# Performance work log

Measured on AMD Instinct MI355X. Metric: run time of the kernel, lower is better.

Reference implementation:

```python
import jax, jax.numpy as jnp
import numpy as np

N_ELEC = 64
IN_C = 64
HID = [64, 128]
OUT_C = 128
BATCH = 2048
BN_EPS = 1e-5


def build_graph():
    """Replicates EEGGraphNet._build_graph_structure with random 3D electrode positions."""
    rng = np.random.RandomState(0)
    pos = rng.rand(N_ELEC, 3).astype(np.float64)
    d = np.sqrt(((pos[:, None, :] - pos[None, :, :]) ** 2).sum(-1))
    thr = np.percentile(d[d > 0], 30)
    src, dst = [], []
    for i in range(N_ELEC):
        for j in range(i + 1, N_ELEC):
            if d[i, j] < thr:
                src += [i, j]
                dst += [j, i]
    return np.asarray(src, np.int32), np.asarray(dst, np.int32)


def setup_inputs() -> dict:
    key = jax.random.key(0)
    ks = jax.random.split(key, 8)
    src, dst = build_graph()
    dims = [IN_C] + HID + [OUT_C]  # [64, 64, 128, 128]
    inp = {"x": jax.random.normal(ks[0], (BATCH, N_ELEC, IN_C), jnp.float32)}
    for li in range(3):
        fi, fo = dims[li], dims[li + 1]
        inp[f"W{li+1}"] = jax.random.normal(ks[li + 1], (fi, fo), jnp.float32) * (1.0 / np.sqrt(fi))
        inp[f"b{li+1}"] = jnp.zeros((fo,), jnp.float32)
    for li in range(2):  # BN after first two convs
        inp[f"g{li+1}"] = jnp.ones((dims[li + 1],), jnp.float32)
        inp[f"be{li+1}"] = jnp.zeros((dims[li + 1],), jnp.float32)
    inp["src"] = jnp.asarray(src)
    inp["dst"] = jnp.asarray(dst)
    return inp


def gcn_conv(x, W, b, src, dst, edge_norm, self_norm):
    # x: (B, N, Fin) -> (B, N, Fout). GCN with self-loops, symmetric norm.
    h = jnp.einsum("bnf,fo->bno", x, W)
    msg = h[:, src, :] * edge_norm[None, :, None]          # (B, E, Fout) gather
    agg = jnp.zeros_like(h).at[:, dst, :].add(msg)         # scatter-add over dst
    return agg + h * self_norm[None, :, None] + b


def batchnorm(x, g, be):
    # torch BatchNorm1d over flattened (B*N, C) nodes, training-mode batch stats
    m = jnp.mean(x, axis=(0, 1))
    v = jnp.mean((x - m) ** 2, axis=(0, 1))
    return g * (x - m) * jax.lax.rsqrt(v + BN_EPS) + be


def reference(x, W1, b1, W2, b2, W3, b3, g1, be1, g2, be2, src, dst):
    # degree (with self-loop) is identical across graphs in the batch
    deg = jnp.zeros((N_ELEC,), x.dtype).at[dst].add(1.0) + 1.0
    inv_sqrt = jax.lax.rsqrt(deg)
    edge_norm = inv_sqrt[src] * inv_sqrt[dst]
    self_norm = 1.0 / deg

    h = gcn_conv(x, W1, b1, src, dst, edge_norm, self_norm)
    h = jax.nn.relu(batchnorm(h, g1, be1))
    h = gcn_conv(h, W2, b2, src, dst, edge_norm, self_norm)
    h = jax.nn.relu(batchnorm(h, g2, be2))
    h = gcn_conv(h, W3, b3, src, dst, edge_norm, self_norm)
    return jnp.mean(h, axis=1)  # global mean pool over electrodes -> (B, OUT_C)
```

## Files before the change

### kernel.cpp

```cpp
#include <hip/hip_runtime.h>
#include <hip/hip_bf16.h>

typedef unsigned short ushortT;
typedef unsigned int uintT;
typedef __attribute__((ext_vector_type(8))) short short8;
typedef __attribute__((ext_vector_type(4))) float f32x4;

#define BATCH   2048
#define NELEC   64
#define BN_EPS  1e-5f

#define OFF_AMEAN  4096
#define OFF_SS1    4160
#define OFF_SS2    4288
#define OFF_PS1    4544
#define OFF_PQ1    8640
#define OFF_PS2    12736
#define OFF_PQ2    20928
#define OFF_ABF    29120
#define OFF_W1T    33216
#define OFF_W2T    37312
#define OFF_H1     45504
#define OFF_T1     4239808
#define OFF_T2     4239808
#define OFF_H2     12628416

#define MFMA(a, b, c) __builtin_amdgcn_mfma_f32_16x16x32_bf16(a, b, c, 0, 0, 0)

__device__ inline float bf2f(ushortT u) { return __uint_as_float(((uintT)u) << 16); }
__device__ inline ushortT f2bf(float f) {
  uintT u = __float_as_uint(f);
  u = (u + 0x7FFFu + ((u >> 16) & 1u)) >> 16;
  return (ushortT)u;
}
__device__ inline void split2(float f, ushortT& hi, ushortT& lo) {
  hi = f2bf(f);
  lo = f2bf(f - bf2f(hi));
}
__device__ inline void splitT8(const float* f, short8& hi, short8& lo) {
  #pragma unroll
  for (int e = 0; e < 8; ++e) {
    uintT u = __float_as_uint(f[e]);
    float fh = __uint_as_float(u & 0xFFFF0000u);
    hi[e] = (short)(u >> 16);
    lo[e] = (short)f2bf(f[e] - fh);
  }
}

__global__ __launch_bounds__(256) void prep_kernel(const int* __restrict__ src,
    const int* __restrict__ dst, int E,
    const float* __restrict__ W1, const float* __restrict__ W2,
    float* __restrict__ ws) {
  __shared__ float degS[NELEC];
  __shared__ float As[NELEC * NELEC];
  int t = threadIdx.x;
  if (t < NELEC) degS[t] = 1.0f;
  for (int i = t; i < NELEC * NELEC; i += 256) As[i] = 0.0f;
  __syncthreads();
  for (int e = t; e < E; e += 256) atomicAdd(&degS[dst[e]], 1.0f);
  __syncthreads();
  for (int e = t; e < E; e += 256) {
    float en = rsqrtf(degS[src[e]]) * rsqrtf(degS[dst[e]]);
    atomicAdd(&As[dst[e] * NELEC + src[e]], en);
  }
  __syncthreads();
  if (t < NELEC) As[t * NELEC + t] += 1.0f / degS[t];
  __syncthreads();
  ushortT* abf = (ushortT*)(ws + OFF_ABF);
  for (int i = t; i < 4096; i += 256) {
    ushortT hi, lo; split2(As[i], hi, lo);
    abf[i] = hi; abf[4096 + i] = lo;
  }
  if (t < NELEC) {
    float s = 0.0f;
    for (int n = 0; n < NELEC; ++n) s += As[n * NELEC + t];
    ws[OFF_AMEAN + t] = s * (1.0f / NELEC);
  }
  ushortT* w1t = (ushortT*)(ws + OFF_W1T);
  for (int i = t; i < 4096; i += 256) {
    int o = i >> 6, k = i & 63;
    ushortT hi, lo; split2(W1[k * 64 + o], hi, lo);
    w1t[i] = hi; w1t[4096 + i] = lo;
  }
  ushortT* w2t = (ushortT*)(ws + OFF_W2T);
  for (int i = t; i < 8192; i += 256) {
    int o = i >> 6, k = i & 63;
    ushortT hi, lo; split2(W2[k * 128 + o], hi, lo);
    w2t[i] = hi; w2t[8192 + i] = lo;
  }
}

__global__ __launch_bounds__(256) void wgemm1_kernel(const float* __restrict__ x,
    float* __restrict__ ws) {
  const int t = threadIdx.x, w = t >> 6, lane = t & 63;
  const int c = lane & 15, g = lane >> 4;
  const int b = blockIdx.x * 4 + w;
  const ushortT* w1t = (const ushortT*)(ws + OFF_W1T);
  ushortT* t1 = (ushortT*)(ws + OFF_T1) + (size_t)b * 4096;

  short8 Xh[4][2], Xl[4][2];
  #pragma unroll
  for (int rt = 0; rt < 4; ++rt) {
    #pragma unroll
    for (int ks = 0; ks < 2; ++ks) {
      const float* p = x + (size_t)b * 4096 + (rt * 16 + c) * 64 + ks * 32 + g * 8;
      float4 fa = *(const float4*)p, fb = *(const float4*)(p + 4);
      float f[8] = {fa.x, fa.y, fa.z, fa.w, fb.x, fb.y, fb.z, fb.w};
      splitT8(f, Xh[rt][ks], Xl[rt][ks]);
    }
  }
  #pragma unroll
  for (int s = 0; s < 4; ++s) {
    f32x4 acc[4] = {{0,0,0,0},{0,0,0,0},{0,0,0,0},{0,0,0,0}};
    #pragma unroll
    for (int ks = 0; ks < 2; ++ks) {
      short8 bh = *(const short8*)(w1t + (s * 16 + c) * 64 + ks * 32 + g * 8);
      short8 bl = *(const short8*)(w1t + 4096 + (s * 16 + c) * 64 + ks * 32 + g * 8);
      #pragma unroll
      for (int rt = 0; rt < 4; ++rt) {
        acc[rt] = MFMA(Xh[rt][ks], bh, acc[rt]);
        acc[rt] = MFMA(Xh[rt][ks], bl, acc[rt]);
        acc[rt] = MFMA(Xl[rt][ks], bh, acc[rt]);
      }
    }
    #pragma unroll
    for (int rt = 0; rt < 4; ++rt) {
      uint2 pk;
      pk.x = (uintT)f2bf(acc[rt][0]) | ((uintT)f2bf(acc[rt][1]) << 16);
      pk.y = (uintT)f2bf(acc[rt][2]) | ((uintT)f2bf(acc[rt][3]) << 16);
      *(uint2*)(t1 + (s * 16 + c) * 64 + rt * 16 + 4 * g) = pk;
    }
  }
}

__global__ __launch_bounds__(256) void agemm1_kernel(const float* __restrict__ b1,
    float* __restrict__ ws) {
  const int t = threadIdx.x, w = t >> 6, lane = t & 63;
  const int c = lane & 15, g = lane >> 4;
  const int wg = blockIdx.x * 4 + w;
  const int ns = wg & 3;
  const int b0 = (wg >> 2) * 2;
  const ushortT* abf = (const ushortT*)(ws + OFF_ABF);
  short8 Bh[2], Bl[2];
  #pragma unroll
  for (int ks = 0; ks < 2; ++ks) {
    Bh[ks] = *(const short8*)(abf + (ns * 16 + c) * 64 + ks * 32 + g * 8);
    Bl[ks] = *(const short8*)(abf + 4096 + (ns * 16 + c) * 64 + ks * 32 + g * 8);
  }
  float Sa[4][4] = {}, Qa[4][4] = {};
  #pragma unroll
  for (int ib = 0; ib < 2; ++ib) {
    const int b = b0 + ib;
    const ushortT* t1 = (const ushortT*)(ws + OFF_T1) + (size_t)b * 4096;
    ushortT* h1 = (ushortT*)(ws + OFF_H1) + (size_t)b * 4096;
    #pragma unroll
    for (int rt = 0; rt < 4; ++rt) {
      f32x4 acc = {0, 0, 0, 0};
      #pragma unroll
      for (int ks = 0; ks < 2; ++ks) {
        short8 tf = *(const short8*)(t1 + (rt * 16 + c) * 64 + ks * 32 + g * 8);
        acc = MFMA(tf, Bh[ks], acc);
        acc = MFMA(tf, Bl[ks], acc);
      }
      float4 bv = *(const float4*)(b1 + rt * 16 + 4 * g);
      float v0 = acc[0] + bv.x, v1 = acc[1] + bv.y;
      float v2 = acc[2] + bv.z, v3 = acc[3] + bv.w;
      Sa[rt][0] += v0; Qa[rt][0] += v0 * v0;
      Sa[rt][1] += v1; Qa[rt][1] += v1 * v1;
      Sa[rt][2] += v2; Qa[rt][2] += v2 * v2;
      Sa[rt][3] += v3; Qa[rt][3] += v3 * v3;
      uint2 pk;
      pk.x = (uintT)f2bf(v0) | ((uintT)f2bf(v1) << 16);
      pk.y = (uintT)f2bf(v2) | ((uintT)f2bf(v3) << 16);
      *(uint2*)(h1 + (ns * 16 + c) * 64 + rt * 16 + 4 * g) = pk;
    }
  }
  const int slot = blockIdx.x & 63;
  #pragma unroll
  for (int rt = 0; rt < 4; ++rt) {
    #pragma unroll
    for (int r = 0; r < 4; ++r) {
      float S = Sa[rt][r], Q = Qa[rt][r];
      S += __shfl_xor(S, 1); S += __shfl_xor(S, 2);
      S += __shfl_xor(S, 4); S += __shfl_xor(S, 8);
      Q += __shfl_xor(Q, 1); Q += __shfl_xor(Q, 2);
      Q += __shfl_xor(Q, 4); Q += __shfl_xor(Q, 8);
      if (c == 0) {
        const int ch = rt * 16 + 4 * g + r;
        atomicAdd(&ws[OFF_PS1 + slot * 64 + ch], S);
        atomicAdd(&ws[OFF_PQ1 + slot * 64 + ch], Q);
      }
    }
  }
}

__global__ void reduce1_kernel(const float* __restrict__ g1, const float* __restrict__ be1,
                               float* __restrict__ ws) {
  int t = threadIdx.x;
  if (t < 64) {
    float S = 0.0f, Q = 0.0f;
    for (int s = 0; s < 64; ++s) { S += ws[OFF_PS1 + s * 64 + t]; Q += ws[OFF_PQ1 + s * 64 + t]; }
    const float inv = 1.0f / (float)(BATCH * NELEC);
    float m = S * inv;
    float v = fmaxf(Q * inv - m * m, 0.0f);
    float sc = g1[t] * rsqrtf(v + BN_EPS);
    ws[OFF_SS1 + t] = sc;
    ws[OFF_SS1 + 64 + t] = fmaf(-m, sc, be1[t]);
  }
}

__global__ void reduce2_kernel(const float* __restrict__ g2, const float* __restrict__ be2,
                               float* __restrict__ ws) {
  int t = threadIdx.x;
  if (t < 128) {
    float S = 0.0f, Q = 0.0f;
    for (int s = 0; s < 64; ++s) { S += ws[OFF_PS2 + s * 128 + t]; Q += ws[OFF_PQ2 + s * 128 + t]; }
    const float inv = 1.0f / (float)(BATCH * NELEC);
    float m = S * inv;
    float v = fmaxf(Q * inv - m * m, 0.0f);
    float sc = g2[t] * rsqrtf(v + BN_EPS);
    ws[OFF_SS2 + t] = sc;
    ws[OFF_SS2 + 128 + t] = fmaf(-m, sc, be2[t]);
  }
}

__global__ __launch_bounds__(256) void wgemm2_kernel(float* __restrict__ ws) {
  const int t = threadIdx.x, w = t >> 6, lane = t & 63;
  const int c = lane & 15, g = lane >> 4;
  const int b = blockIdx.x * 4 + w;
  const ushortT* w2t = (const ushortT*)(ws + OFF_W2T);
  const ushortT* h1 = (const ushortT*)(ws + OFF_H1) + (size_t)b * 4096;
  ushortT* t2 = (ushortT*)(ws + OFF_T2) + (size_t)b * 8192;

  float s1v[2][8], t1v[2][8];
  #pragma unroll
  for (int ks = 0; ks < 2; ++ks) {
    const float* sp = ws + OFF_SS1 + ks * 32 + g * 8;
    const float* tp = ws + OFF_SS1 + 64 + ks * 32 + g * 8;
    float4 sa = *(const float4*)sp, sb = *(const float4*)(sp + 4);
    float4 ta = *(const float4*)tp, tb = *(const float4*)(tp + 4);
    s1v[ks][0]=sa.x; s1v[ks][1]=sa.y; s1v[ks][2]=sa.z; s1v[ks][3]=sa.w;
    s1v[ks][4]=sb.x; s1v[ks][5]=sb.y; s1v[ks][6]=sb.z; s1v[ks][7]=sb.w;
    t1v[ks][0]=ta.x; t1v[ks][1]=ta.y; t1v[ks][2]=ta.z; t1v[ks][3]=ta.w;
    t1v[ks][4]=tb.x; t1v[ks][5]=tb.y; t1v[ks][6]=tb.z; t1v[ks][7]=tb.w;
  }
  short8 Yh[4][2], Yl[4][2];
  #pragma unroll
  for (int rt = 0; rt < 4; ++rt) {
    #pragma unroll
    for (int ks = 0; ks < 2; ++ks) {
      short8 hv = *(const short8*)(h1 + (rt * 16 + c) * 64 + ks * 32 + g * 8);
      float f[8];
      #pragma unroll
      for (int e = 0; e < 8; ++e)
        f[e] = fmaxf(fmaf(bf2f((ushortT)hv[e]), s1v[ks][e], t1v[ks][e]), 0.0f);
      splitT8(f, Yh[rt][ks], Yl[rt][ks]);
    }
  }
  #pragma unroll
  for (int s = 0; s < 8; ++s) {
    f32x4 acc[4] = {{0,0,0,0},{0,0,0,0},{0,0,0,0},{0,0,0,0}};
    #pragma unroll
    for (int ks = 0; ks < 2; ++ks) {
      short8 bh = *(const short8*)(w2t + (s * 16 + c) * 64 + ks * 32 + g * 8);
      short8 bl = *(const short8*)(w2t + 8192 + (s * 16 + c) * 64 + ks * 32 + g * 8);
      #pragma unroll
      for (int rt = 0; rt < 4; ++rt) {
        acc[rt] = MFMA(Yh[rt][ks], bh, acc[rt]);
        acc[rt] = MFMA(Yh[rt][ks], bl, acc[rt]);
        acc[rt] = MFMA(Yl[rt][ks], bh, acc[rt]);
      }
    }
    #pragma unroll
    for (int rt = 0; rt < 4; ++rt) {
      uint2 pk;
      pk.x = (uintT)f2bf(acc[rt][0]) | ((uintT)f2bf(acc[rt][1]) << 16);
      pk.y = (uintT)f2bf(acc[rt][2]) | ((uintT)f2bf(acc[rt][3]) << 16);
      *(uint2*)(t2 + (s * 16 + c) * 64 + rt * 16 + 4 * g) = pk;
    }
  }
}

__global__ __launch_bounds__(256) void agemm2_kernel(const float* __restrict__ b2,
    float* __restrict__ ws) {
  const int t = threadIdx.x, w = t >> 6, lane = t & 63;
  const int c = lane & 15, g = lane >> 4;
  const int wg = blockIdx.x * 4 + w;
  const int ns = wg & 3;
  const int b0 = (wg >> 2) * 2;
  const ushortT* abf = (const ushortT*)(ws + OFF_ABF);
  short8 Bh[2], Bl[2];
  #pragma unroll
  for (int ks = 0; ks < 2; ++ks) {
    Bh[ks] = *(const short8*)(abf + (ns * 16 + c) * 64 + ks * 32 + g * 8);
    Bl[ks] = *(const short8*)(abf + 4096 + (ns * 16 + c) * 64 + ks * 32 + g * 8);
  }
  float Sa[8][4] = {}, Qa[8][4] = {};
  #pragma unroll
  for (int ib = 0; ib < 2; ++ib) {
    const int b = b0 + ib;
    const ushortT* t2 = (const ushortT*)(ws + OFF_T2) + (size_t)b * 8192;
    ushortT* h2 = (ushortT*)(ws + OFF_H2) + (size_t)b * 8192;
    #pragma unroll
    for (int rt = 0; rt < 8; ++rt) {
      f32x4 acc = {0, 0, 0, 0};
      #pragma unroll
      for (int ks = 0; ks < 2; ++ks) {
        short8 tf = *(const short8*)(t2 + (rt * 16 + c) * 64 + ks * 32 + g * 8);
        acc = MFMA(tf, Bh[ks], acc);
        acc = MFMA(tf, Bl[ks], acc);
      }
      float4 bv = *(const float4*)(b2 + rt * 16 + 4 * g);
      float v0 = acc[0] + bv.x, v1 = acc[1] + bv.y;
      float v2 = acc[2] + bv.z, v3 = acc[3] + bv.w;
      Sa[rt][0] += v0; Qa[rt][0] += v0 * v0;
      Sa[rt][1] += v1; Qa[rt][1] += v1 * v1;
      Sa[rt][2] += v2; Qa[rt][2] += v2 * v2;
      Sa[rt][3] += v3; Qa[rt][3] += v3 * v3;
      uint2 pk;
      pk.x = (uintT)f2bf(v0) | ((uintT)f2bf(v1) << 16);
      pk.y = (uintT)f2bf(v2) | ((uintT)f2bf(v3) << 16);
      *(uint2*)(h2 + (ns * 16 + c) * 128 + rt * 16 + 4 * g) = pk;
    }
  }
  const int slot = blockIdx.x & 63;
  #pragma unroll
  for (int rt = 0; rt < 8; ++rt) {
    #pragma unroll
    for (int r = 0; r < 4; ++r) {
      float S = Sa[rt][r], Q = Qa[rt][r];
      S += __shfl_xor(S, 1); S += __shfl_xor(S, 2);
      S += __shfl_xor(S, 4); S += __shfl_xor(S, 8);
      Q += __shfl_xor(Q, 1); Q += __shfl_xor(Q, 2);
      Q += __shfl_xor(Q, 4); Q += __shfl_xor(Q, 8);
      if (c == 0) {
        const int ch = rt * 16 + 4 * g + r;
        atomicAdd(&ws[OFF_PS2 + slot * 128 + ch], S);
        atomicAdd(&ws[OFF_PQ2 + slot * 128 + ch], Q);
      }
    }
  }
}

__global__ __launch_bounds__(256) void layer3_kernel(const float* __restrict__ W3,
    const float* __restrict__ b3, const float* __restrict__ ws,
    float* __restrict__ out) {
  const int w = threadIdx.x >> 6, lane = threadIdx.x & 63;
  const int item = blockIdx.x * 4 + w;
  const int f0 = lane * 2;
  const float s2a = ws[OFF_SS2 + f0],       s2b = ws[OFF_SS2 + f0 + 1];
  const float t2a = ws[OFF_SS2 + 128 + f0], t2b = ws[OFF_SS2 + 128 + f0 + 1];
  const float* am = ws + OFF_AMEAN;
  const ushortT* h2 = (const ushortT*)(ws + OFF_H2) + (size_t)item * 8192;
  float v0 = 0.0f, v1 = 0.0f;
  #pragma unroll 8
  for (int m = 0; m < 64; ++m) {
    uintT pk = *(const uintT*)(h2 + m * 128 + f0);
    float y0 = fmaxf(fmaf(bf2f((ushortT)(pk & 0xffffu)), s2a, t2a), 0.0f);
    float y1 = fmaxf(fmaf(bf2f((ushortT)(pk >> 16)),     s2b, t2b), 0.0f);
    float a = am[m];
    v0 = fmaf(a, y0, v0);
    v1 = fmaf(a, y1, v1);
  }
  float o0 = b3[f0], o1 = b3[f0 + 1];
  #pragma unroll 8
  for (int k = 0; k < 128; ++k) {
    float vk = __shfl((k & 1) ? v1 : v0, k >> 1, 64);
    o0 = fmaf(vk, W3[k * 128 + f0],     o0);
    o1 = fmaf(vk, W3[k * 128 + f0 + 1], o1);
  }
  float2 ov; ov.x = o0; ov.y = o1;
  *(float2*)(out + (size_t)item * 128 + f0) = ov;
}

extern "C" void kernel_launch(void* const* d_in, const int* in_sizes, int n_in,
                              void* d_out, int out_size, void* d_ws, size_t ws_size,
                              hipStream_t stream) {
  const float* x   = (const float*)d_in[0];
  const float* W1  = (const float*)d_in[1];
  const float* b1  = (const float*)d_in[2];
  const float* W2  = (const float*)d_in[3];
  const float* b2  = (const float*)d_in[4];
  const float* W3  = (const float*)d_in[5];
  const float* b3  = (const float*)d_in[6];
  const float* g1  = (const float*)d_in[7];
  const float* be1 = (const float*)d_in[8];
  const float* g2  = (const float*)d_in[9];
  const float* be2 = (const float*)d_in[10];
  const int*   src = (const int*)d_in[11];
  const int*   dst = (const int*)d_in[12];
  const int E = in_sizes[11];
  float* ws  = (float*)d_ws;
  float* out = (float*)d_out;

  hipMemsetAsync((void*)(ws + OFF_PS1), 0, (size_t)(29120 - OFF_PS1) * 4, stream);
  hipLaunchKernelGGL(prep_kernel,   dim3(1),    dim3(256), 0, stream, src, dst, E, W1, W2, ws);
  hipLaunchKernelGGL(wgemm1_kernel, dim3(512),  dim3(256), 0, stream, x, ws);
  hipLaunchKernelGGL(agemm1_kernel, dim3(1024), dim3(256), 0, stream, b1, ws);
  hipLaunchKernelGGL(reduce1_kernel,dim3(1),    dim3(64),  0, stream, g1, be1, ws);
  hipLaunchKernelGGL(wgemm2_kernel, dim3(512),  dim3(256), 0, stream, ws);
  hipLaunchKernelGGL(agemm2_kernel, dim3(1024), dim3(256), 0, stream, b2, ws);
  hipLaunchKernelGGL(reduce2_kernel,dim3(1),    dim3(128), 0, stream, g2, be2, ws);
  hipLaunchKernelGGL(layer3_kernel, dim3(512),  dim3(256), 0, stream, W3, b3, ws, out);
}
```

Before: 225.0 us.

## Fuse weight GEMM and adjacency GEMM per layer through LDS staging

Merges the separate weight-GEMM and adjacency-GEMM kernels of layers 1 and 2 into single kernels. The intermediate X·W tile now stays in padded shared memory instead of going through global memory. Weights are loaded into LDS once per block, and operand layouts are padded to a row stride of 72 (136 for the H2 staging) to avoid bank conflicts. H1 and H2 are written back with coalesced 16-byte stores from LDS. This removes two kernel launches and a large global round-trip of the intermediates. In exchange it uses heavy LDS per block, which may limit occupancy.

```diff
diff --git a/kernel.cpp b/kernel.cpp
--- a/kernel.cpp
+++ b/kernel.cpp
@@ -17,13 +17,11 @@
 #define OFF_PQ1    8640
 #define OFF_PS2    12736
 #define OFF_PQ2    20928
-#define OFF_ABF    29120
-#define OFF_W1T    33216
-#define OFF_W2T    37312
-#define OFF_H1     45504
-#define OFF_T1     4239808
-#define OFF_T2     4239808
-#define OFF_H2     12628416
+#define UOFF_A     0
+#define UOFF_W1T   9216
+#define UOFF_W2T   18432
+#define UOFF_H1    36864
+#define UOFF_H2    (36864 + 8388608)
 
 #define MFMA(a, b, c) __builtin_amdgcn_mfma_f32_16x16x32_bf16(a, b, c, 0, 0, 0)
 
@@ -45,6 +43,12 @@
     hi[e] = (short)(u >> 16);
     lo[e] = (short)f2bf(f[e] - fh);
   }
+}
+__device__ inline uint2 pack4(f32x4 v) {
+  uint2 pk;
+  pk.x = (uintT)f2bf(v[0]) | ((uintT)f2bf(v[1]) << 16);
+  pk.y = (uintT)f2bf(v[2]) | ((uintT)f2bf(v[3]) << 16);
+  return pk;
 }
 
 __global__ __launch_bounds__(256) void prep_kernel(const int* __restrict__ src,
@@ -66,131 +70,146 @@
   __syncthreads();
   if (t < NELEC) As[t * NELEC + t] += 1.0f / degS[t];
   __syncthreads();
-  ushortT* abf = (ushortT*)(ws + OFF_ABF);
+  ushortT* U = (ushortT*)(ws + 29120);
+  ushortT* a72 = U + UOFF_A;
   for (int i = t; i < 4096; i += 256) {
+    int row = i >> 6, k = i & 63;
     ushortT hi, lo; split2(As[i], hi, lo);
-    abf[i] = hi; abf[4096 + i] = lo;
+    a72[row * 72 + k] = hi; a72[4608 + row * 72 + k] = lo;
   }
   if (t < NELEC) {
     float s = 0.0f;
     for (int n = 0; n < NELEC; ++n) s += As[n * NELEC + t];
     ws[OFF_AMEAN + t] = s * (1.0f / NELEC);
   }
-  ushortT* w1t = (ushortT*)(ws + OFF_W1T);
+  ushortT* w1t = U + UOFF_W1T;
   for (int i = t; i < 4096; i += 256) {
     int o = i >> 6, k = i & 63;
     ushortT hi, lo; split2(W1[k * 64 + o], hi, lo);
-    w1t[i] = hi; w1t[4096 + i] = lo;
-  }
-  ushortT* w2t = (ushortT*)(ws + OFF_W2T);
+    w1t[o * 72 + k] = hi; w1t[4608 + o * 72 + k] = lo;
+  }
+  ushortT* w2t = U + UOFF_W2T;
   for (int i = t; i < 8192; i += 256) {
     int o = i >> 6, k = i & 63;
     ushortT hi, lo; split2(W2[k * 128 + o], hi, lo);
-    w2t[i] = hi; w2t[8192 + i] = lo;
-  }
-}
-
-__global__ __launch_bounds__(256) void wgemm1_kernel(const float* __restrict__ x,
-    float* __restrict__ ws) {
-  const int t = threadIdx.x, w = t >> 6, lane = t & 63;
-  const int c = lane & 15, g = lane >> 4;
-  const int b = blockIdx.x * 4 + w;
-  const ushortT* w1t = (const ushortT*)(ws + OFF_W1T);
-  ushortT* t1 = (ushortT*)(ws + OFF_T1) + (size_t)b * 4096;
-
+    w2t[o * 72 + k] = hi; w2t[9216 + o * 72 + k] = lo;
+  }
+}
+
+__global__ __launch_bounds__(512, 2) void layer1_fused(const float* __restrict__ x,
+    const float* __restrict__ b1, float* __restrict__ ws) {
+  __shared__ ushortT Wl[9216];
+  __shared__ ushortT Tt[36864];
+  const int t = threadIdx.x;
+  ushortT* U = (ushortT*)(ws + 29120);
+  for (int i = t; i < 1152; i += 512)
+    ((uint4*)Wl)[i] = ((const uint4*)(U + UOFF_W1T))[i];
+  const int w = t >> 6, lane = t & 63, c = lane & 15, g = lane >> 4;
+  const int b = blockIdx.x * 8 + w;
   short8 Xh[4][2], Xl[4][2];
   #pragma unroll
-  for (int rt = 0; rt < 4; ++rt) {
-    #pragma unroll
-    for (int ks = 0; ks < 2; ++ks) {
-      const float* p = x + (size_t)b * 4096 + (rt * 16 + c) * 64 + ks * 32 + g * 8;
+  for (int nq = 0; nq < 4; ++nq) {
+    #pragma unroll
+    for (int ks = 0; ks < 2; ++ks) {
+      const float* p = x + (size_t)b * 4096 + (nq * 16 + c) * 64 + ks * 32 + g * 8;
       float4 fa = *(const float4*)p, fb = *(const float4*)(p + 4);
       float f[8] = {fa.x, fa.y, fa.z, fa.w, fb.x, fb.y, fb.z, fb.w};
-      splitT8(f, Xh[rt][ks], Xl[rt][ks]);
-    }
-  }
-  #pragma unroll
-  for (int s = 0; s < 4; ++s) {
-    f32x4 acc[4] = {{0,0,0,0},{0,0,0,0},{0,0,0,0},{0,0,0,0}};
-    #pragma unroll
-    for (int ks = 0; ks < 2; ++ks) {
-      short8 bh = *(const short8*)(w1t + (s * 16 + c) * 64 + ks * 32 + g * 8);
-      short8 bl = *(const short8*)(w1t + 4096 + (s * 16 + c) * 64 + ks * 32 + g * 8);
+      splitT8(f, Xh[nq][ks], Xl[nq][ks]);
+    }
+  }
+  __syncthreads();
+  f32x4 acc[4][4];
+  #pragma unroll
+  for (int i = 0; i < 4; ++i)
+    #pragma unroll
+    for (int j = 0; j < 4; ++j) acc[i][j] = (f32x4){0.f, 0.f, 0.f, 0.f};
+  #pragma unroll
+  for (int ot = 0; ot < 4; ++ot) {
+    #pragma unroll
+    for (int ks = 0; ks < 2; ++ks) {
+      short8 bh = *(const short8*)&Wl[(ot * 16 + c) * 72 + ks * 32 + g * 8];
+      short8 bl = *(const short8*)&Wl[4608 + (ot * 16 + c) * 72 + ks * 32 + g * 8];
+      #pragma unroll
+      for (int nq = 0; nq < 4; ++nq) {
+        acc[nq][ot] = MFMA(Xh[nq][ks], bh, acc[nq][ot]);
+        acc[nq][ot] = MFMA(Xh[nq][ks], bl, acc[nq][ot]);
+        acc[nq][ot] = MFMA(Xl[nq][ks], bh, acc[nq][ot]);
+      }
+    }
+  }
+  ushortT* tt = &Tt[w * 4608];
+  #pragma unroll
+  for (int ot = 0; ot < 4; ++ot)
+    #pragma unroll
+    for (int nq = 0; nq < 4; ++nq)
+      *(uint2*)&tt[(ot * 16 + c) * 72 + nq * 16 + 4 * g] = pack4(acc[nq][ot]);
+  short8 ABh[4][2], ABl[4][2];
+  #pragma unroll
+  for (int sp = 0; sp < 4; ++sp)
+    #pragma unroll
+    for (int ks = 0; ks < 2; ++ks) {
+      ABh[sp][ks] = *(const short8*)(U + (sp * 16 + c) * 72 + ks * 32 + g * 8);
+      ABl[sp][ks] = *(const short8*)(U + 4608 + (sp * 16 + c) * 72 + ks * 32 + g * 8);
+    }
+  f32x4 h[4][4];
+  #pragma unroll
+  for (int i = 0; i < 4; ++i)
+    #pragma unroll
+    for (int j = 0; j < 4; ++j) h[i][j] = (f32x4){0.f, 0.f, 0.f, 0.f};
+  #pragma unroll
+  for (int ks = 0; ks < 2; ++ks) {
+    short8 af[4];
+    #pragma unroll
+    for (int rt = 0; rt < 4; ++rt)
+      af[rt] = *(const short8*)&tt[(rt * 16 + c) * 72 + ks * 32 + g * 8];
+    #pragma unroll
+    for (int sp = 0; sp < 4; ++sp)
       #pragma unroll
       for (int rt = 0; rt < 4; ++rt) {
-        acc[rt] = MFMA(Xh[rt][ks], bh, acc[rt]);
-        acc[rt] = MFMA(Xh[rt][ks], bl, acc[rt]);
-        acc[rt] = MFMA(Xl[rt][ks], bh, acc[rt]);
-      }
-    }
-    #pragma unroll
-    for (int rt = 0; rt < 4; ++rt) {
-      uint2 pk;
-      pk.x = (uintT)f2bf(acc[rt][0]) | ((uintT)f2bf(acc[rt][1]) << 16);
-      pk.y = (uintT)f2bf(acc[rt][2]) | ((uintT)f2bf(acc[rt][3]) << 16);
-      *(uint2*)(t1 + (s * 16 + c) * 64 + rt * 16 + 4 * g) = pk;
-    }
-  }
-}
-
-__global__ __launch_bounds__(256) void agemm1_kernel(const float* __restrict__ b1,
-    float* __restrict__ ws) {
-  const int t = threadIdx.x, w = t >> 6, lane = t & 63;
-  const int c = lane & 15, g = lane >> 4;
-  const int wg = blockIdx.x * 4 + w;
-  const int ns = wg & 3;
-  const int b0 = (wg >> 2) * 2;
-  const ushortT* abf = (const ushortT*)(ws + OFF_ABF);
-  short8 Bh[2], Bl[2];
-  #pragma unroll
-  for (int ks = 0; ks < 2; ++ks) {
-    Bh[ks] = *(const short8*)(abf + (ns * 16 + c) * 64 + ks * 32 + g * 8);
-    Bl[ks] = *(const short8*)(abf + 4096 + (ns * 16 + c) * 64 + ks * 32 + g * 8);
-  }
-  float Sa[4][4] = {}, Qa[4][4] = {};
-  #pragma unroll
-  for (int ib = 0; ib < 2; ++ib) {
-    const int b = b0 + ib;
-    const ushortT* t1 = (const ushortT*)(ws + OFF_T1) + (size_t)b * 4096;
-    ushortT* h1 = (ushortT*)(ws + OFF_H1) + (size_t)b * 4096;
-    #pragma unroll
-    for (int rt = 0; rt < 4; ++rt) {
-      f32x4 acc = {0, 0, 0, 0};
-      #pragma unroll
-      for (int ks = 0; ks < 2; ++ks) {
-        short8 tf = *(const short8*)(t1 + (rt * 16 + c) * 64 + ks * 32 + g * 8);
-        acc = MFMA(tf, Bh[ks], acc);
-        acc = MFMA(tf, Bl[ks], acc);
-      }
-      float4 bv = *(const float4*)(b1 + rt * 16 + 4 * g);
-      float v0 = acc[0] + bv.x, v1 = acc[1] + bv.y;
-      float v2 = acc[2] + bv.z, v3 = acc[3] + bv.w;
-      Sa[rt][0] += v0; Qa[rt][0] += v0 * v0;
-      Sa[rt][1] += v1; Qa[rt][1] += v1 * v1;
-      Sa[rt][2] += v2; Qa[rt][2] += v2 * v2;
-      Sa[rt][3] += v3; Qa[rt][3] += v3 * v3;
-      uint2 pk;
-      pk.x = (uintT)f2bf(v0) | ((uintT)f2bf(v1) << 16);
-      pk.y = (uintT)f2bf(v2) | ((uintT)f2bf(v3) << 16);
-      *(uint2*)(h1 + (ns * 16 + c) * 64 + rt * 16 + 4 * g) = pk;
+        h[rt][sp] = MFMA(af[rt], ABh[sp][ks], h[rt][sp]);
+        h[rt][sp] = MFMA(af[rt], ABl[sp][ks], h[rt][sp]);
+      }
+  }
+  float Sa[4][4], Qa[4][4];
+  #pragma unroll
+  for (int i = 0; i < 4; ++i)
+    #pragma unroll
+    for (int j = 0; j < 4; ++j) { Sa[i][j] = 0.f; Qa[i][j] = 0.f; }
+  #pragma unroll
+  for (int rt = 0; rt < 4; ++rt) {
+    float4 bv = *(const float4*)(b1 + rt * 16 + 4 * g);
+    #pragma unroll
+    for (int sp = 0; sp < 4; ++sp) {
+      f32x4 v;
+      v[0] = h[rt][sp][0] + bv.x; v[1] = h[rt][sp][1] + bv.y;
+      v[2] = h[rt][sp][2] + bv.z; v[3] = h[rt][sp][3] + bv.w;
+      Sa[rt][0] += v[0]; Qa[rt][0] += v[0] * v[0];
+      Sa[rt][1] += v[1]; Qa[rt][1] += v[1] * v[1];
+      Sa[rt][2] += v[2]; Qa[rt][2] += v[2] * v[2];
+      Sa[rt][3] += v[3]; Qa[rt][3] += v[3] * v[3];
+      *(uint2*)&tt[(sp * 16 + c) * 72 + rt * 16 + 4 * g] = pack4(v);
     }
   }
   const int slot = blockIdx.x & 63;
   #pragma unroll
-  for (int rt = 0; rt < 4; ++rt) {
+  for (int rt = 0; rt < 4; ++rt)
     #pragma unroll
     for (int r = 0; r < 4; ++r) {
       float S = Sa[rt][r], Q = Qa[rt][r];
-      S += __shfl_xor(S, 1); S += __shfl_xor(S, 2);
-      S += __shfl_xor(S, 4); S += __shfl_xor(S, 8);
-      Q += __shfl_xor(Q, 1); Q += __shfl_xor(Q, 2);
-      Q += __shfl_xor(Q, 4); Q += __shfl_xor(Q, 8);
+      S += __shfl_xor(S, 1); S += __shfl_xor(S, 2); S += __shfl_xor(S, 4); S += __shfl_xor(S, 8);
+      Q += __shfl_xor(Q, 1); Q += __shfl_xor(Q, 2); Q += __shfl_xor(Q, 4); Q += __shfl_xor(Q, 8);
       if (c == 0) {
-        const int ch = rt * 16 + 4 * g + r;
-        atomicAdd(&ws[OFF_PS1 + slot * 64 + ch], S);
-        atomicAdd(&ws[OFF_PQ1 + slot * 64 + ch], Q);
-      }
-    }
+        atomicAdd(&ws[OFF_PS1 + slot * 64 + rt * 16 + 4 * g + r], S);
+        atomicAdd(&ws[OFF_PQ1 + slot * 64 + rt * 16 + 4 * g + r], Q);
+      }
+    }
+  __syncthreads();
+  {
+    const int ib = t >> 6, n2 = t & 63;
+    const uint4* srcp = (const uint4*)&Tt[ib * 4608 + n2 * 72];
+    uint4* dstp = (uint4*)(U + UOFF_H1 + (size_t)(blockIdx.x * 8 + ib) * 4096 + n2 * 64);
+    #pragma unroll
+    for (int j = 0; j < 8; ++j) dstp[j] = srcp[j];
   }
 }
 
@@ -224,121 +243,148 @@
   }
 }
 
-__global__ __launch_bounds__(256) void wgemm2_kernel(float* __restrict__ ws) {
-  const int t = threadIdx.x, w = t >> 6, lane = t & 63;
-  const int c = lane & 15, g = lane >> 4;
-  const int b = blockIdx.x * 4 + w;
-  const ushortT* w2t = (const ushortT*)(ws + OFF_W2T);
-  const ushortT* h1 = (const ushortT*)(ws + OFF_H1) + (size_t)b * 4096;
-  ushortT* t2 = (ushortT*)(ws + OFF_T2) + (size_t)b * 8192;
-
-  float s1v[2][8], t1v[2][8];
+__global__ __launch_bounds__(512, 2) void layer2_fused(const float* __restrict__ b2,
+    float* __restrict__ ws) {
+  __shared__ ushortT Wl[18432];
+  __shared__ ushortT Tt[36864];
+  const int t = threadIdx.x;
+  ushortT* U = (ushortT*)(ws + 29120);
+  for (int i = t; i < 2304; i += 512)
+    ((uint4*)Wl)[i] = ((const uint4*)(U + UOFF_W2T))[i];
+  const int w = t >> 6, lane = t & 63, c = lane & 15, g = lane >> 4;
+  const int b0 = blockIdx.x * 4;
+  const ushortT* h1g = U + UOFF_H1;
+  float s8[2][8], t8[2][8];
   #pragma unroll
   for (int ks = 0; ks < 2; ++ks) {
-    const float* sp = ws + OFF_SS1 + ks * 32 + g * 8;
-    const float* tp = ws + OFF_SS1 + 64 + ks * 32 + g * 8;
-    float4 sa = *(const float4*)sp, sb = *(const float4*)(sp + 4);
-    float4 ta = *(const float4*)tp, tb = *(const float4*)(tp + 4);
-    s1v[ks][0]=sa.x; s1v[ks][1]=sa.y; s1v[ks][2]=sa.z; s1v[ks][3]=sa.w;
-    s1v[ks][4]=sb.x; s1v[ks][5]=sb.y; s1v[ks][6]=sb.z; s1v[ks][7]=sb.w;
-    t1v[ks][0]=ta.x; t1v[ks][1]=ta.y; t1v[ks][2]=ta.z; t1v[ks][3]=ta.w;
-    t1v[ks][4]=tb.x; t1v[ks][5]=tb.y; t1v[ks][6]=tb.z; t1v[ks][7]=tb.w;
-  }
-  short8 Yh[4][2], Yl[4][2];
+    const float* sp_ = ws + OFF_SS1 + ks * 32 + g * 8;
+    const float* tp_ = ws + OFF_SS1 + 64 + ks * 32 + g * 8;
+    float4 sa = *(const float4*)sp_, sb = *(const float4*)(sp_ + 4);
+    float4 ta = *(const float4*)tp_, tb = *(const float4*)(tp_ + 4);
+    s8[ks][0]=sa.x; s8[ks][1]=sa.y; s8[ks][2]=sa.z; s8[ks][3]=sa.w;
+    s8[ks][4]=sb.x; s8[ks][5]=sb.y; s8[ks][6]=sb.z; s8[ks][7]=sb.w;
+    t8[ks][0]=ta.x; t8[ks][1]=ta.y; t8[ks][2]=ta.z; t8[ks][3]=ta.w;
+    t8[ks][4]=tb.x; t8[ks][5]=tb.y; t8[ks][6]=tb.z; t8[ks][7]=tb.w;
+  }
+  short8 Yh[2][2], Yl[2][2];
+  #pragma unroll
+  for (int si = 0; si < 2; ++si) {
+    const int sub = w * 2 + si, ib = sub >> 2, nq = sub & 3;
+    #pragma unroll
+    for (int ks = 0; ks < 2; ++ks) {
+      short8 hv = *(const short8*)(h1g + (size_t)(b0 + ib) * 4096 + (nq * 16 + c) * 64 + ks * 32 + g * 8);
+      float f[8];
+      #pragma unroll
+      for (int e = 0; e < 8; ++e)
+        f[e] = fmaxf(fmaf(bf2f((ushortT)hv[e]), s8[ks][e], t8[ks][e]), 0.0f);
+      splitT8(f, Yh[si][ks], Yl[si][ks]);
+    }
+  }
+  __syncthreads();
+  f32x4 acc[2][8];
+  #pragma unroll
+  for (int i = 0; i < 2; ++i)
+    #pragma unroll
+    for (int j = 0; j < 8; ++j) acc[i][j] = (f32x4){0.f, 0.f, 0.f, 0.f};
+  #pragma unroll
+  for (int ot = 0; ot < 8; ++ot) {
+    #pragma unroll
+    for (int ks = 0; ks < 2; ++ks) {
+      short8 bh = *(const short8*)&Wl[(ot * 16 + c) * 72 + ks * 32 + g * 8];
+      short8 bl = *(const short8*)&Wl[9216 + (ot * 16 + c) * 72 + ks * 32 + g * 8];
+      #pragma unroll
+      for (int si = 0; si < 2; ++si) {
+        acc[si][ot] = MFMA(Yh[si][ks], bh, acc[si][ot]);
+        acc[si][ot] = MFMA(Yh[si][ks], bl, acc[si][ot]);
+        acc[si][ot] = MFMA(Yl[si][ks], bh, acc[si][ot]);
+      }
+    }
+  }
+  #pragma unroll
+  for (int si = 0; si < 2; ++si) {
+    const int sub = w * 2 + si, ib = sub >> 2, nq = sub & 3;
+    #pragma unroll
+    for (int ot = 0; ot < 8; ++ot)
+      *(uint2*)&Tt[ib * 9216 + (ot * 16 + c) * 72 + nq * 16 + 4 * g] = pack4(acc[si][ot]);
+  }
+  short8 ABh[4][2], ABl[4][2];
+  #pragma unroll
+  for (int sp = 0; sp < 4; ++sp)
+    #pragma unroll
+    for (int ks = 0; ks < 2; ++ks) {
+      ABh[sp][ks] = *(const short8*)(U + (sp * 16 + c) * 72 + ks * 32 + g * 8);
+      ABl[sp][ks] = *(const short8*)(U + 4608 + (sp * 16 + c) * 72 + ks * 32 + g * 8);
+    }
+  __syncthreads();
+  const int ib = w >> 1, oh = w & 1;
+  const ushortT* tt = &Tt[ib * 9216];
+  f32x4 h[4][4];
+  #pragma unroll
+  for (int i = 0; i < 4; ++i)
+    #pragma unroll
+    for (int j = 0; j < 4; ++j) h[i][j] = (f32x4){0.f, 0.f, 0.f, 0.f};
+  #pragma unroll
+  for (int ks = 0; ks < 2; ++ks) {
+    short8 af[4];
+    #pragma unroll
+    for (int rt = 0; rt < 4; ++rt)
+      af[rt] = *(const short8*)&tt[(oh * 64 + rt * 16 + c) * 72 + ks * 32 + g * 8];
+    #pragma unroll
+    for (int sp = 0; sp < 4; ++sp)
+      #pragma unroll
+      for (int rt = 0; rt < 4; ++rt) {
+        h[rt][sp] = MFMA(af[rt], ABh[sp][ks], h[rt][sp]);
+        h[rt][sp] = MFMA(af[rt], ABl[sp][ks], h[rt][sp]);
+      }
+  }
+  float Sa[4][4], Qa[4][4];
+  #pragma unroll
+  for (int i = 0; i < 4; ++i)
+    #pragma unroll
+    for (int j = 0; j < 4; ++j) { Sa[i][j] = 0.f; Qa[i][j] = 0.f; }
   #pragma unroll
   for (int rt = 0; rt < 4; ++rt) {
-    #pragma unroll
-    for (int ks = 0; ks < 2; ++ks) {
-      short8 hv = *(const short8*)(h1 + (rt * 16 + c) * 64 + ks * 32 + g * 8);
-      float f[8];
-      #pragma unroll
-      for (int e = 0; e < 8; ++e)
-        f[e] = fmaxf(fmaf(bf2f((ushortT)hv[e]), s1v[ks][e], t1v[ks][e]), 0.0f);
-      splitT8(f, Yh[rt][ks], Yl[rt][ks]);
-    }
-  }
-  #pragma unroll
-  for (int s = 0; s < 8; ++s) {
-    f32x4 acc[4] = {{0,0,0,0},{0,0,0,0},{0,0,0,0},{0,0,0,0}};
-    #pragma unroll
-    for (int ks = 0; ks < 2; ++ks) {
-      short8 bh = *(const short8*)(w2t + (s * 16 + c) * 64 + ks * 32 + g * 8);
-      short8 bl = *(const short8*)(w2t + 8192 + (s * 16 + c) * 64 + ks * 32 + g * 8);
-      #pragma unroll
-      for (int rt = 0; rt < 4; ++rt) {
-        acc[rt] = MFMA(Yh[rt][ks], bh, acc[rt]);
-        acc[rt] = MFMA(Yh[rt][ks], bl, acc[rt]);
-        acc[rt] = MFMA(Yl[rt][ks], bh, acc[rt]);
-      }
-    }
-    #pragma unroll
-    for (int rt = 0; rt < 4; ++rt) {
-      uint2 pk;
-      pk.x = (uintT)f2bf(acc[rt][0]) | ((uintT)f2bf(acc[rt][1]) << 16);
-      pk.y = (uintT)f2bf(acc[rt][2]) | ((uintT)f2bf(acc[rt][3]) << 16);
-      *(uint2*)(t2 + (s * 16 + c) * 64 + rt * 16 + 4 * g) = pk;
-    }
-  }
-}
-
-__global__ __launch_bounds__(256) void agemm2_kernel(const float* __restrict__ b2,
-    float* __restrict__ ws) {
-  const int t = threadIdx.x, w = t >> 6, lane = t & 63;
-  const int c = lane & 15, g = lane >> 4;
-  const int wg = blockIdx.x * 4 + w;
-  const int ns = wg & 3;
-  const int b0 = (wg >> 2) * 2;
-  const ushortT* abf = (const ushortT*)(ws + OFF_ABF);
-  short8 Bh[2], Bl[2];
-  #pragma unroll
-  for (int ks = 0; ks < 2; ++ks) {
-    Bh[ks] = *(const short8*)(abf + (ns * 16 + c) * 64 + ks * 32 + g * 8);
-    Bl[ks] = *(const short8*)(abf + 4096 + (ns * 16 + c) * 64 + ks * 32 + g * 8);
-  }
-  float Sa[8][4] = {}, Qa[8][4] = {};
-  #pragma unroll
-  for (int ib = 0; ib < 2; ++ib) {
-    const int b = b0 + ib;
-    const ushortT* t2 = (const ushortT*)(ws + OFF_T2) + (size_t)b * 8192;
-    ushortT* h2 = (ushortT*)(ws + OFF_H2) + (size_t)b * 8192;
-    #pragma unroll
-    for (int rt = 0; rt < 8; ++rt) {
-      f32x4 acc = {0, 0, 0, 0};
-      #pragma unroll
-      for (int ks = 0; ks < 2; ++ks) {
-        short8 tf = *(const short8*)(t2 + (rt * 16 + c) * 64 + ks * 32 + g * 8);
-        acc = MFMA(tf, Bh[ks], acc);
-        acc = MFMA(tf, Bl[ks], acc);
-      }
-      float4 bv = *(const float4*)(b2 + rt * 16 + 4 * g);
-      float v0 = acc[0] + bv.x, v1 = acc[1] + bv.y;
-      float v2 = acc[2] + bv.z, v3 = acc[3] + bv.w;
-      Sa[rt][0] += v0; Qa[rt][0] += v0 * v0;
-      Sa[rt][1] += v1; Qa[rt][1] += v1 * v1;
-      Sa[rt][2] += v2; Qa[rt][2] += v2 * v2;
-      Sa[rt][3] += v3; Qa[rt][3] += v3 * v3;
-      uint2 pk;
-      pk.x = (uintT)f2bf(v0) | ((uintT)f2bf(v1) << 16);
-      pk.y = (uintT)f2bf(v2) | ((uintT)f2bf(v3) << 16);
-      *(uint2*)(h2 + (ns * 16 + c) * 128 + rt * 16 + 4 * g) = pk;
+    float4 bv = *(const float4*)(b2 + oh * 64 + rt * 16 + 4 * g);
+    #pragma unroll
+    for (int sp = 0; sp < 4; ++sp) {
+      h[rt][sp][0] += bv.x; h[rt][sp][1] += bv.y;
+      h[rt][sp][2] += bv.z; h[rt][sp][3] += bv.w;
+      Sa[rt][0] += h[rt][sp][0]; Qa[rt][0] += h[rt][sp][0] * h[rt][sp][0];
+      Sa[rt][1] += h[rt][sp][1]; Qa[rt][1] += h[rt][sp][1] * h[rt][sp][1];
+      Sa[rt][2] += h[rt][sp][2]; Qa[rt][2] += h[rt][sp][2] * h[rt][sp][2];
+      Sa[rt][3] += h[rt][sp][3]; Qa[rt][3] += h[rt][sp][3] * h[rt][sp][3];
     }
   }
   const int slot = blockIdx.x & 63;
   #pragma unroll
-  for (int rt = 0; rt < 8; ++rt) {
+  for (int rt = 0; rt < 4; ++rt)
     #pragma unroll
     for (int r = 0; r < 4; ++r) {
       float S = Sa[rt][r], Q = Qa[rt][r];
-      S += __shfl_xor(S, 1); S += __shfl_xor(S, 2);
-      S += __shfl_xor(S, 4); S += __shfl_xor(S, 8);
-      Q += __shfl_xor(Q, 1); Q += __shfl_xor(Q, 2);
-      Q += __shfl_xor(Q, 4); Q += __shfl_xor(Q, 8);
+      S += __shfl_xor(S, 1); S += __shfl_xor(S, 2); S += __shfl_xor(S, 4); S += __shfl_xor(S, 8);
+      Q += __shfl_xor(Q, 1); Q += __shfl_xor(Q, 2); Q += __shfl_xor(Q, 4); Q += __shfl_xor(Q, 8);
       if (c == 0) {
-        const int ch = rt * 16 + 4 * g + r;
+        const int ch = oh * 64 + rt * 16 + 4 * g + r;
         atomicAdd(&ws[OFF_PS2 + slot * 128 + ch], S);
         atomicAdd(&ws[OFF_PQ2 + slot * 128 + ch], Q);
       }
     }
+  __syncthreads();
+  {
+    ushortT* hb = &Tt[ib * 9216];
+    #pragma unroll
+    for (int rt = 0; rt < 4; ++rt)
+      #pragma unroll
+      for (int sp = 0; sp < 4; ++sp)
+        *(uint2*)&hb[(sp * 16 + c) * 136 + oh * 64 + rt * 16 + 4 * g] = pack4(h[rt][sp]);
+  }
+  __syncthreads();
+  {
+    const int ib2 = t >> 7, n2 = (t >> 1) & 63, half = t & 1;
+    const uint4* srcp = (const uint4*)&Tt[ib2 * 9216 + n2 * 136 + half * 64];
+    uint4* dstp = (uint4*)(U + UOFF_H2 + (size_t)(b0 + ib2) * 8192 + n2 * 128 + half * 64);
+    #pragma unroll
+    for (int j = 0; j < 8; ++j) dstp[j] = srcp[j];
   }
 }
 
@@ -351,7 +397,7 @@
   const float s2a = ws[OFF_SS2 + f0],       s2b = ws[OFF_SS2 + f0 + 1];
   const float t2a = ws[OFF_SS2 + 128 + f0], t2b = ws[OFF_SS2 + 128 + f0 + 1];
   const float* am = ws + OFF_AMEAN;
-  const ushortT* h2 = (const ushortT*)(ws + OFF_H2) + (size_t)item * 8192;
+  const ushortT* h2 = (const ushortT*)(ws + 29120) + UOFF_H2 + (size_t)item * 8192;
   float v0 = 0.0f, v1 = 0.0f;
   #pragma unroll 8
   for (int m = 0; m < 64; ++m) {
@@ -394,12 +440,10 @@
   float* out = (float*)d_out;
 
   hipMemsetAsync((void*)(ws + OFF_PS1), 0, (size_t)(29120 - OFF_PS1) * 4, stream);
-  hipLaunchKernelGGL(prep_kernel,   dim3(1),    dim3(256), 0, stream, src, dst, E, W1, W2, ws);
-  hipLaunchKernelGGL(wgemm1_kernel, dim3(512),  dim3(256), 0, stream, x, ws);
-  hipLaunchKernelGGL(agemm1_kernel, dim3(1024), dim3(256), 0, stream, b1, ws);
-  hipLaunchKernelGGL(reduce1_kernel,dim3(1),    dim3(64),  0, stream, g1, be1, ws);
-  hipLaunchKernelGGL(wgemm2_kernel, dim3(512),  dim3(256), 0, stream, ws);
-  hipLaunchKernelGGL(agemm2_kernel, dim3(1024), dim3(256), 0, stream, b2, ws);
-  hipLaunchKernelGGL(reduce2_kernel,dim3(1),    dim3(128), 0, stream, g2, be2, ws);
-  hipLaunchKernelGGL(layer3_kernel, dim3(512),  dim3(256), 0, stream, W3, b3, ws, out);
-}
+  hipLaunchKernelGGL(prep_kernel,    dim3(1),   dim3(256), 0, stream, src, dst, E, W1, W2, ws);
+  hipLaunchKernelGGL(layer1_fused,   dim3(256), dim3(512), 0, stream, x, b1, ws);
+  hipLaunchKernelGGL(reduce1_kernel, dim3(1),   dim3(64),  0, stream, g1, be1, ws);
+  hipLaunchKernelGGL(layer2_fused,   dim3(512), dim3(512), 0, stream, b2, ws);
+  hipLaunchKernelGGL(reduce2_kernel, dim3(1),   dim3(128), 0, stream, g2, be2, ws);
+  hipLaunchKernelGGL(layer3_kernel,  dim3(512), dim3(256), 0, stream, W3, b3, ws, out);
+}
```

Result: faster. 186.2 us (-17.3%).
